# Kernel optimization log

Hardware: AMD Instinct MI355X
Metric: run time of the kernel (lower is better)

The kernel has to match this reference:

```python
import jax, jax.numpy as jnp
import numpy as np

QMAX = 127.0  # int8 symmetric range per get_quant_min_max(torch.int8)


def setup_inputs() -> dict:
    key = jax.random.key(0)
    k1, k2, k3, k4, k5, k6 = jax.random.split(key, 6)
    B, S, IN, OUT = 4, 2048, 4096, 4096
    x = jax.random.normal(k1, (B, S, IN), dtype=jnp.float32)
    # smoothquant-style per-input-channel scale (1/scale in torch code), positive
    input_scale = jax.random.uniform(k2, (IN,), jnp.float32, 0.5, 2.0)
    # per-tensor static activation scale (positive scalar)
    act_scale = jax.random.uniform(k3, (), jnp.float32, 0.01, 0.03)
    # pre-quantized int8 weight values in [-127, 127], stored as int32
    w_int = jax.random.randint(k4, (OUT, IN), -127, 128, dtype=jnp.int32)
    # per-out-channel weight scale
    w_scale = jax.random.uniform(k5, (OUT,), jnp.float32, 0.001, 0.01)
    bias = jax.random.normal(k6, (OUT,), dtype=jnp.float32) * 0.1
    return {"x": x, "input_scale": input_scale, "act_scale": act_scale,
            "w_int": w_int, "w_scale": w_scale, "bias": bias}


def reference(x, input_scale, act_scale, w_int, w_scale, bias):
    # mode == 'quantized' path of QModule.forward with forward_module = F.linear
    # 1) smooth-scale activations, 2) static affine int8 quantize (zero_point NONE)
    xs = x * input_scale  # [B,S,IN]
    xi = jnp.clip(jnp.round(xs / act_scale), -QMAX, QMAX).astype(jnp.int32)
    # 3) integer matmul (exact, matches torch double matmul of int values + round)
    acc = jnp.einsum('bsi,oi->bso', xi, w_int)  # int32 accumulate, exact
    # 4) dequant: scale = q(q(scale_i * scale_w, f32), f32) -> plain f32 product here
    scale = act_scale * w_scale  # [OUT]
    out = acc.astype(jnp.float32) * scale + bias
    return out
```

## Files before the change

kernel.cpp:

```cpp
#include <hip/hip_runtime.h>
#include <hip/hip_bf16.h>
#include <stdint.h>

#define Mdim 8192
#define Ndim 4096
#define Kdim 4096

#define BM 256
#define BN 256
#define BK 128

typedef int v4i __attribute__((ext_vector_type(4)));

__device__ __forceinline__ void gload_lds16(const void* g, void* l) {
  __builtin_amdgcn_global_load_lds(
      (const __attribute__((address_space(1))) unsigned int*)g,
      (__attribute__((address_space(3))) unsigned int*)l,
      16 , 0 , 0 );
}

__global__ void quant_x_kernel(const float* __restrict__ x,
                               const float* __restrict__ in_scale,
                               const float* __restrict__ act_scale_p,
                               int8_t* __restrict__ xq) {
  const float inv_act = 1.0f / (*act_scale_p);
  const int64_t tid = (int64_t)blockIdx.x * blockDim.x + threadIdx.x;
  const int64_t base = tid * 16;
  const int k0 = (int)(base & (Kdim - 1));
  const float4* xv = (const float4*)(x + base);
  const float4* sv = (const float4*)(in_scale + k0);
  alignas(16) int8_t ob[16];
#pragma unroll
  for (int j = 0; j < 4; ++j) {
    float4 xx = xv[j];
    float4 ss = sv[j];
    float r0 = rintf((xx.x * ss.x) * inv_act);
    float r1 = rintf((xx.y * ss.y) * inv_act);
    float r2 = rintf((xx.z * ss.z) * inv_act);
    float r3 = rintf((xx.w * ss.w) * inv_act);
    r0 = fminf(fmaxf(r0, -127.f), 127.f);
    r1 = fminf(fmaxf(r1, -127.f), 127.f);
    r2 = fminf(fmaxf(r2, -127.f), 127.f);
    r3 = fminf(fmaxf(r3, -127.f), 127.f);
    ob[j * 4 + 0] = (int8_t)r0;
    ob[j * 4 + 1] = (int8_t)r1;
    ob[j * 4 + 2] = (int8_t)r2;
    ob[j * 4 + 3] = (int8_t)r3;
  }
  *(v4i*)(xq + base) = *(const v4i*)ob;
}

__global__ void pack_w_kernel(const int* __restrict__ w, int8_t* __restrict__ wq) {
  const int64_t tid = (int64_t)blockIdx.x * blockDim.x + threadIdx.x;
  const int64_t base = tid * 16;
  const int4* wv = (const int4*)(w + base);
  alignas(16) int8_t ob[16];
#pragma unroll
  for (int j = 0; j < 4; ++j) {
    int4 t = wv[j];
    ob[j * 4 + 0] = (int8_t)t.x;
    ob[j * 4 + 1] = (int8_t)t.y;
    ob[j * 4 + 2] = (int8_t)t.z;
    ob[j * 4 + 3] = (int8_t)t.w;
  }
  *(v4i*)(wq + base) = *(const v4i*)ob;
}

#define PBAR()                        \
  do {                                \
    asm volatile("" ::: "memory");    \
    __builtin_amdgcn_s_barrier();     \
    asm volatile("" ::: "memory");    \
  } while (0)
#define LGKM0() asm volatile("s_waitcnt lgkmcnt(0)" ::: "memory")
#define VMCNT(n) asm volatile("s_waitcnt vmcnt(" #n ")" ::: "memory")

#define MFMA16(mh)                                                        \
  do {                                                                    \
    __builtin_amdgcn_s_setprio(1);                                        \
    _Pragma("unroll") for (int i = 0; i < 4; ++i) {                       \
      _Pragma("unroll") for (int j = 0; j < 4; ++j) {                     \
        acc[(mh) * 4 + i][j] = __builtin_amdgcn_mfma_i32_16x16x64_i8(     \
            af[i], bf[j], acc[(mh) * 4 + i][j], 0, 0, 0);                 \
      }                                                                   \
    }                                                                     \
    __builtin_amdgcn_s_setprio(0);                                        \
  } while (0)

__global__ __launch_bounds__(512, 2) void gemm_i8_kernel(
    const int8_t* __restrict__ Aq, const int8_t* __restrict__ Bq,
    const float* __restrict__ w_scale, const float* __restrict__ bias,
    const float* __restrict__ act_scale_p, float* __restrict__ out) {
  __shared__ alignas(16) int8_t As[2][2][BM * 64];
  __shared__ alignas(16) int8_t Bs[2][2][BN * 64];

  const int t = threadIdx.x;

  const int lin = blockIdx.x;
  const int within = lin & 31;
  const int m_blk = (lin >> 5) * 2 + (within & 1);
  const int n_blk = within >> 1;
  const int m0 = m_blk * BM;
  const int n0 = n_blk * BN;

  const int srow = t >> 2;
  const int scol = ((t & 3) ^ ((t >> 3) & 3)) * 16;
  const int8_t* gA0 = Aq + (int64_t)(m0 + srow) * Kdim + scol;
  const int8_t* gA1 = gA0 + (int64_t)128 * Kdim;
  const int8_t* gB0 = Bq + (int64_t)(n0 + srow) * Kdim + scol;
  const int8_t* gB1 = gB0 + (int64_t)128 * Kdim;
  const int ldst = t * 16;

  const int w = t >> 6;
  const int l = t & 63;
  const int wm = (w >> 2) * 128;
  const int wn = (w & 3) * 64;
  const int lrow = l & 15;
  const int lk = ((l >> 4) ^ ((l >> 1) & 3)) * 16;
  const int abase = (wm + lrow) * 64 + lk;
  const int bbase = (wn + lrow) * 64 + lk;

  v4i acc[8][4] = {};

#define STG(MAT, buf, ks, h, koff) \
  gload_lds16(g##MAT##h + (koff) + (ks) * 64, &MAT##s[buf][ks][(h) * 8192 + ldst])

  STG(A, 0, 0, 0, 0); STG(B, 0, 0, 0, 0);
  STG(A, 0, 0, 1, 0); STG(B, 0, 0, 1, 0);
  STG(A, 0, 1, 0, 0); STG(B, 0, 1, 0, 0);
  STG(A, 0, 1, 1, 0); STG(B, 0, 1, 1, 0);
  VMCNT(4);
  PBAR();

  for (int kt = 0; kt < Kdim; kt += BK) {
    const int cur = (kt >> 7) & 1;
    const int nxt = cur ^ 1;
    int kn = kt + BK;
    if (kn >= Kdim) kn = 0;

    v4i af[4], bf[4];

#pragma unroll
    for (int j = 0; j < 4; ++j) bf[j] = *(const v4i*)&Bs[cur][0][bbase + j * 1024];
#pragma unroll
    for (int i = 0; i < 4; ++i) af[i] = *(const v4i*)&As[cur][0][abase + i * 1024];
    STG(A, nxt, 0, 0, kn); STG(B, nxt, 0, 0, kn);
    PBAR(); LGKM0();
    MFMA16(0);
    PBAR();

#pragma unroll
    for (int i = 0; i < 4; ++i) af[i] = *(const v4i*)&As[cur][0][abase + 4096 + i * 1024];
    STG(A, nxt, 0, 1, kn); STG(B, nxt, 0, 1, kn);
    PBAR(); LGKM0();
    MFMA16(1);
    VMCNT(4);
    PBAR();

#pragma unroll
    for (int j = 0; j < 4; ++j) bf[j] = *(const v4i*)&Bs[cur][1][bbase + j * 1024];
#pragma unroll
    for (int i = 0; i < 4; ++i) af[i] = *(const v4i*)&As[cur][1][abase + i * 1024];
    STG(A, nxt, 1, 0, kn); STG(B, nxt, 1, 0, kn);
    PBAR(); LGKM0();
    MFMA16(0);
    PBAR();

#pragma unroll
    for (int i = 0; i < 4; ++i) af[i] = *(const v4i*)&As[cur][1][abase + 4096 + i * 1024];
    STG(A, nxt, 1, 1, kn); STG(B, nxt, 1, 1, kn);
    PBAR(); LGKM0();
    MFMA16(1);
    VMCNT(4);
    PBAR();
  }
  VMCNT(0);

  const float act = *act_scale_p;
  const int rowbase = (l >> 4) * 4;
#pragma unroll
  for (int j = 0; j < 4; ++j) {
    const int n = n0 + wn + j * 16 + lrow;
    const float sc = act * w_scale[n];
    const float bs = bias[n];
#pragma unroll
    for (int i = 0; i < 8; ++i) {
      const int mb = m0 + wm + i * 16 + rowbase;
#pragma unroll
      for (int r = 0; r < 4; ++r) {
        out[(int64_t)(mb + r) * Ndim + n] = (float)acc[i][j][r] * sc + bs;
      }
    }
  }
}

extern "C" void kernel_launch(void* const* d_in, const int* in_sizes, int n_in,
                              void* d_out, int out_size, void* d_ws, size_t ws_size,
                              hipStream_t stream) {
  const float* x        = (const float*)d_in[0];
  const float* in_scale = (const float*)d_in[1];
  const float* actp     = (const float*)d_in[2];
  const int*   w_int    = (const int*)d_in[3];
  const float* w_scale  = (const float*)d_in[4];
  const float* bias     = (const float*)d_in[5];
  float* out = (float*)d_out;

  int8_t* Aq = (int8_t*)d_ws;
  int8_t* Bq = (int8_t*)d_ws + (size_t)Mdim * Kdim;

  {
    const int64_t nthreads = (int64_t)Mdim * Kdim / 16;
    quant_x_kernel<<<(int)(nthreads / 256), 256, 0, stream>>>(x, in_scale, actp, Aq);
  }
  {
    const int64_t nthreads = (int64_t)Ndim * Kdim / 16;
    pack_w_kernel<<<(int)(nthreads / 256), 256, 0, stream>>>(w_int, Bq);
  }
  {
    gemm_i8_kernel<<<dim3(512), 512, 0, stream>>>(Aq, Bq, w_scale, bias, actp, out);
  }
}
```

Baseline: 403.2 us.

## Replace double-buffered K tiles with three-slot ring of 64-wide K slices

The GEMM main loop now walks K in 64-wide slices through a three-entry LDS ring, prefetching two slices ahead, instead of double-buffered 128-wide tiles. It drops most per-phase barriers and explicit lgkmcnt waits, leaving one vmcnt wait and one barrier per slice. The aim is to cut synchronization stalls and overlap global-to-LDS copies with MFMA work. The LDS footprint shrinks from 128KB to 96KB. Correctness now depends on the compiler inserting the LDS read waits, since the explicit ones were removed.

```diff
diff --git a/kernel.cpp b/kernel.cpp
--- a/kernel.cpp
+++ b/kernel.cpp
@@ -8,7 +8,7 @@
 
 #define BM 256
 #define BN 256
-#define BK 128
+#define NSLICE (Kdim / 64)
 
 typedef int v4i __attribute__((ext_vector_type(4)));
 
@@ -72,27 +72,14 @@
     __builtin_amdgcn_s_barrier();     \
     asm volatile("" ::: "memory");    \
   } while (0)
-#define LGKM0() asm volatile("s_waitcnt lgkmcnt(0)" ::: "memory")
 #define VMCNT(n) asm volatile("s_waitcnt vmcnt(" #n ")" ::: "memory")
-
-#define MFMA16(mh)                                                        \
-  do {                                                                    \
-    __builtin_amdgcn_s_setprio(1);                                        \
-    _Pragma("unroll") for (int i = 0; i < 4; ++i) {                       \
-      _Pragma("unroll") for (int j = 0; j < 4; ++j) {                     \
-        acc[(mh) * 4 + i][j] = __builtin_amdgcn_mfma_i32_16x16x64_i8(     \
-            af[i], bf[j], acc[(mh) * 4 + i][j], 0, 0, 0);                 \
-      }                                                                   \
-    }                                                                     \
-    __builtin_amdgcn_s_setprio(0);                                        \
-  } while (0)
 
 __global__ __launch_bounds__(512, 2) void gemm_i8_kernel(
     const int8_t* __restrict__ Aq, const int8_t* __restrict__ Bq,
     const float* __restrict__ w_scale, const float* __restrict__ bias,
     const float* __restrict__ act_scale_p, float* __restrict__ out) {
-  __shared__ alignas(16) int8_t As[2][2][BM * 64];
-  __shared__ alignas(16) int8_t Bs[2][2][BN * 64];
+  __shared__ alignas(16) int8_t As[3][BM * 64];
+  __shared__ alignas(16) int8_t Bs[3][BN * 64];
 
   const int t = threadIdx.x;
 
@@ -122,57 +109,61 @@
 
   v4i acc[8][4] = {};
 
-#define STG(MAT, buf, ks, h, koff) \
-  gload_lds16(g##MAT##h + (koff) + (ks) * 64, &MAT##s[buf][ks][(h) * 8192 + ldst])
-
-  STG(A, 0, 0, 0, 0); STG(B, 0, 0, 0, 0);
-  STG(A, 0, 0, 1, 0); STG(B, 0, 0, 1, 0);
-  STG(A, 0, 1, 0, 0); STG(B, 0, 1, 0, 0);
-  STG(A, 0, 1, 1, 0); STG(B, 0, 1, 1, 0);
+#define STG_SLICE(s, r)                              \
+  do {                                               \
+    const int ko_ = (s) * 64;                        \
+    gload_lds16(gA0 + ko_, &As[r][ldst]);            \
+    gload_lds16(gA1 + ko_, &As[r][8192 + ldst]);     \
+    gload_lds16(gB0 + ko_, &Bs[r][ldst]);            \
+    gload_lds16(gB1 + ko_, &Bs[r][8192 + ldst]);     \
+  } while (0)
+
+  STG_SLICE(0, 0);
+  STG_SLICE(1, 1);
   VMCNT(4);
   PBAR();
 
-  for (int kt = 0; kt < Kdim; kt += BK) {
-    const int cur = (kt >> 7) & 1;
-    const int nxt = cur ^ 1;
-    int kn = kt + BK;
-    if (kn >= Kdim) kn = 0;
-
+  int ring = 0;
+  for (int s = 0; s < NSLICE; ++s) {
+    const int r = ring;
+    int rn = ring + 2; if (rn >= 3) rn -= 3;
+    int sp = s + 2; if (sp >= NSLICE) sp -= NSLICE;
+    const int ko = sp * 64;
+
+    const int8_t* Ab = As[r];
+    const int8_t* Bb = Bs[r];
     v4i af[4], bf[4];
 
 #pragma unroll
-    for (int j = 0; j < 4; ++j) bf[j] = *(const v4i*)&Bs[cur][0][bbase + j * 1024];
-#pragma unroll
-    for (int i = 0; i < 4; ++i) af[i] = *(const v4i*)&As[cur][0][abase + i * 1024];
-    STG(A, nxt, 0, 0, kn); STG(B, nxt, 0, 0, kn);
-    PBAR(); LGKM0();
-    MFMA16(0);
-    PBAR();
-
-#pragma unroll
-    for (int i = 0; i < 4; ++i) af[i] = *(const v4i*)&As[cur][0][abase + 4096 + i * 1024];
-    STG(A, nxt, 0, 1, kn); STG(B, nxt, 0, 1, kn);
-    PBAR(); LGKM0();
-    MFMA16(1);
+    for (int j = 0; j < 4; ++j) bf[j] = *(const v4i*)&Bb[bbase + j * 1024];
+#pragma unroll
+    for (int i = 0; i < 4; ++i) af[i] = *(const v4i*)&Ab[abase + i * 1024];
+    gload_lds16(gA0 + ko, &As[rn][ldst]);
+    gload_lds16(gA1 + ko, &As[rn][8192 + ldst]);
+    __builtin_amdgcn_s_setprio(1);
+#pragma unroll
+    for (int i = 0; i < 4; ++i)
+#pragma unroll
+      for (int j = 0; j < 4; ++j)
+        acc[i][j] = __builtin_amdgcn_mfma_i32_16x16x64_i8(af[i], bf[j], acc[i][j], 0, 0, 0);
+    __builtin_amdgcn_s_setprio(0);
+
+#pragma unroll
+    for (int i = 0; i < 4; ++i) af[i] = *(const v4i*)&Ab[abase + 4096 + i * 1024];
+    gload_lds16(gB0 + ko, &Bs[rn][ldst]);
+    gload_lds16(gB1 + ko, &Bs[rn][8192 + ldst]);
+    __builtin_amdgcn_s_setprio(1);
+#pragma unroll
+    for (int i = 0; i < 4; ++i)
+#pragma unroll
+      for (int j = 0; j < 4; ++j)
+        acc[4 + i][j] = __builtin_amdgcn_mfma_i32_16x16x64_i8(af[i], bf[j], acc[4 + i][j], 0, 0, 0);
+    __builtin_amdgcn_s_setprio(0);
+
     VMCNT(4);
     PBAR();
 
-#pragma unroll
-    for (int j = 0; j < 4; ++j) bf[j] = *(const v4i*)&Bs[cur][1][bbase + j * 1024];
-#pragma unroll
-    for (int i = 0; i < 4; ++i) af[i] = *(const v4i*)&As[cur][1][abase + i * 1024];
-    STG(A, nxt, 1, 0, kn); STG(B, nxt, 1, 0, kn);
-    PBAR(); LGKM0();
-    MFMA16(0);
-    PBAR();
-
-#pragma unroll
-    for (int i = 0; i < 4; ++i) af[i] = *(const v4i*)&As[cur][1][abase + 4096 + i * 1024];
-    STG(A, nxt, 1, 1, kn); STG(B, nxt, 1, 1, kn);
-    PBAR(); LGKM0();
-    MFMA16(1);
-    VMCNT(4);
-    PBAR();
+    ring = ring + 1; if (ring >= 3) ring -= 3;
   }
   VMCNT(0);
 
```

New measurement: 415.2 us. +3.0%, slower.
